# Optimization experiments

Hardware: AMD Instinct MI355X
Metric: run time of the kernel (lower is better)

## Reference

```python
import jax, jax.numpy as jnp
import numpy as np

EPS = 1e-5
AVG_LOG = 1.0  # avg_d['log']
N_NODES = 100000
N_EDGES = 1600000
IN_DIM = 64
EDGE_DIM = 16
OUT_DIM = 64


def setup_inputs() -> dict:
    key = jax.random.key(0)
    ks = jax.random.split(key, 12)
    d_pre_in = 2 * IN_DIM + EDGE_DIM           # 144
    d_post_in = (4 * 3 + 1) * IN_DIM           # 13*64 = 832
    inp = {
        "node_feat": jax.random.normal(ks[0], (N_NODES, IN_DIM), jnp.float32),
        "edge_feat": jax.random.normal(ks[1], (N_EDGES, EDGE_DIM), jnp.float32),
        "pre_W": jax.random.normal(ks[2], (d_pre_in, IN_DIM), jnp.float32) / np.sqrt(d_pre_in),
        "pre_b": jnp.zeros((IN_DIM,), jnp.float32),
        "post_W1": jax.random.normal(ks[3], (d_post_in, OUT_DIM), jnp.float32) / np.sqrt(d_post_in),
        "post_b1": jnp.zeros((OUT_DIM,), jnp.float32),
        "bn_gamma": jnp.ones((OUT_DIM,), jnp.float32),
        "bn_beta": jnp.zeros((OUT_DIM,), jnp.float32),
        "post_W2": jax.random.normal(ks[4], (OUT_DIM, OUT_DIM), jnp.float32) / np.sqrt(OUT_DIM),
        "post_b2": jnp.zeros((OUT_DIM,), jnp.float32),
        "src": jax.random.randint(ks[5], (N_EDGES,), 0, N_NODES, jnp.int32),
        "dst": jax.random.randint(ks[6], (N_EDGES,), 0, N_NODES, jnp.int32),
    }
    return inp


def reference(node_feat, edge_feat, pre_W, pre_b, post_W1, post_b1,
              bn_gamma, bn_beta, post_W2, post_b2, src, dst):
    N = node_feat.shape[0]
    h_in = node_feat

    # --- pretrans edge MLP: cat(h_src, h_dst, e_feat) -> Linear -> relu ---
    z = jnp.concatenate([node_feat[src], node_feat[dst], edge_feat], axis=-1)  # [E, 2D+De]
    e = jax.nn.relu(z @ pre_W + pre_b)                                         # [E, D]

    # --- multi-aggregator neighbor reduction (messages flow src->dst) ---
    deg = jax.ops.segment_sum(jnp.ones((src.shape[0],), e.dtype), dst, num_segments=N)  # [N]
    degc = jnp.maximum(deg, 1.0)[:, None]
    s = jax.ops.segment_sum(e, dst, num_segments=N)
    mean = s / degc
    msq = jax.ops.segment_sum(e * e, dst, num_segments=N) / degc
    var = jax.nn.relu(msq - mean * mean)
    std = jnp.sqrt(var + EPS)
    mx = jax.ops.segment_max(e, dst, num_segments=N)
    mn = jax.ops.segment_min(e, dst, num_segments=N)
    has = (deg > 0)[:, None]
    agg = jnp.concatenate([mean, jnp.where(has, mx, 0.0),
                           jnp.where(has, mn, 0.0), std], axis=-1)  # [N, 4D]
    agg = jnp.where(has, agg, 0.0)  # DGL leaves zero-in-degree nodes zero-filled

    # --- degree scalers: identity, amplification, attenuation ---
    logD = jnp.log(deg + 1.0)[:, None]
    amp = agg * (logD / AVG_LOG)
    att = agg * jnp.where(has, AVG_LOG / jnp.maximum(logD, EPS), 0.0)
    scaled = jnp.concatenate([agg, amp, att], axis=-1)  # [N, 12D]

    # --- posttrans MLP: Linear->relu->BN->Linear->relu, + residual ---
    h = jnp.concatenate([h_in, scaled], axis=-1)        # [N, 13D]
    x = jax.nn.relu(h @ post_W1 + post_b1)
    mu = x.mean(axis=0)
    v = ((x - mu) ** 2).mean(axis=0)
    x = bn_gamma * (x - mu) / jnp.sqrt(v + EPS) + bn_beta
    x = jax.nn.relu(x @ post_W2 + post_b2)
    return x + h_in
```

## Files before the change

kernel.cpp:

```cpp
#include <hip/hip_runtime.h>
#include <math.h>

#define EPSF 1e-5f

typedef __attribute__((ext_vector_type(8))) _Float16 h16x8;
typedef __attribute__((ext_vector_type(4))) float f32x4;
typedef __attribute__((ext_vector_type(4))) unsigned short us4;
typedef __attribute__((ext_vector_type(8))) unsigned short us8;

static __device__ __forceinline__ unsigned short f2h(float f) {
  _Float16 h = (_Float16)f;
  return __builtin_bit_cast(unsigned short, h);
}
static __device__ __forceinline__ float h2f(unsigned short u) {
  _Float16 h = __builtin_bit_cast(_Float16, u);
  return (float)h;
}
static __device__ __forceinline__ int ibcast(int v, int l) {
  return __builtin_amdgcn_readlane(v, l);
}
static __device__ __forceinline__ int lanegather(int v, int srcLane) {
  return __builtin_amdgcn_ds_bpermute(srcLane << 2, v);
}


__global__ __launch_bounds__(256) void k_deg(const int* __restrict__ dst,
                                             int* __restrict__ deg,
                                             int* __restrict__ rank, int E) {
  int i = blockIdx.x * 256 + threadIdx.x;
  if (i < E) rank[i] = atomicAdd(&deg[dst[i]], 1);
}

__global__ __launch_bounds__(1024) void k_scan_a(const int* __restrict__ deg,
                                                 int* __restrict__ offs,
                                                 int* __restrict__ bsum,
                                                 float* __restrict__ aux2, int N) {
  __shared__ int s[1024];
  int t = threadIdx.x;
  int i = blockIdx.x * 1024 + t;
  int v = (i < N) ? deg[i] : 0;
  s[t] = v;
  __syncthreads();
  for (int off = 1; off < 1024; off <<= 1) {
    int x = (t >= off) ? s[t - off] : 0;
    __syncthreads();
    s[t] += x;
    __syncthreads();
  }
  if (i < N) {
    offs[i] = s[t] - v;
    float logD = logf((float)v + 1.f);
    aux2[i * 2] = logD;
    aux2[i * 2 + 1] = (v > 0) ? 1.f / fmaxf(logD, EPSF) : 0.f;
  }
  if (t == 1023) bsum[blockIdx.x] = s[1023];
}

__global__ __launch_bounds__(1024) void k_scan_b(int* __restrict__ bsum, int nb) {
  __shared__ int s[1024];
  int t = threadIdx.x;
  int v = (t < nb) ? bsum[t] : 0;
  s[t] = v;
  __syncthreads();
  for (int off = 1; off < 1024; off <<= 1) {
    int x = (t >= off) ? s[t - off] : 0;
    __syncthreads();
    s[t] += x;
    __syncthreads();
  }
  if (t < nb) bsum[t] = s[t] - v;
}

__global__ __launch_bounds__(1024) void k_scan_c(int* __restrict__ offs,
                                                 const int* __restrict__ bsum,
                                                 int N) {
  int i = blockIdx.x * 1024 + threadIdx.x;
  if (i < N) offs[i] += bsum[blockIdx.x];
}


__global__ __launch_bounds__(256) void k_prep(const float* __restrict__ pre_W,
                                              const float* __restrict__ post_W1,
                                              const float* __restrict__ post_W2,
                                              unsigned short* __restrict__ wsdt,
                                              unsigned short* __restrict__ wt2,
                                              unsigned short* __restrict__ wt3) {
  int idx = blockIdx.x * 256 + threadIdx.x;
  if (idx < 128 * 64) {
    int c = idx >> 6, k = idx & 63;
    float v = (c < 64) ? pre_W[k * 64 + c] : pre_W[(64 + k) * 64 + (c - 64)];
    wsdt[idx] = f2h(v);
  }
  int j = idx - 128 * 64;
  if (j >= 0 && j < 192 * 320) {
    int c = j / 320, k = j - c * 320;
    float v;
    if (c < 64) v = post_W1[k * 64 + c];
    else if (c < 128) v = (k < 64) ? 0.f : post_W1[(256 + k) * 64 + (c - 64)];
    else v = (k < 64) ? 0.f : post_W1[(512 + k) * 64 + (c - 128)];
    wt2[j] = f2h(v);
  }
  int m = idx - 128 * 64 - 192 * 320;
  if (m >= 0 && m < 64 * 64) {
    int c = m >> 6, k = m & 63;
    wt3[m] = f2h(post_W2[k * 64 + c]);
  }
}


__global__ __launch_bounds__(256) void kB_proj(
    const float* __restrict__ nf, const unsigned short* __restrict__ wsdt,
    const float* __restrict__ pre_b, unsigned short* __restrict__ ps,
    unsigned short* __restrict__ pd, int N) {
  __shared__ unsigned short at[64][72];
  int tid = threadIdx.x;
  int n0 = blockIdx.x * 64;
  for (int idx = tid; idx < 64 * 16; idx += 256) {
    int row = idx >> 4, s4 = idx & 15;
    int n = n0 + row;
    us4 o = {0, 0, 0, 0};
    if (n < N) {
      f32x4 v = *(const f32x4*)(nf + (long)n * 64 + s4 * 4);
      o.x = f2h(v.x); o.y = f2h(v.y); o.z = f2h(v.z); o.w = f2h(v.w);
    }
    *(us4*)&at[row][s4 * 4] = o;
    if (s4 < 2) { us4 z = {0, 0, 0, 0}; *(us4*)&at[row][64 + s4 * 4] = z; }
  }
  __syncthreads();
  int lane = tid & 63, w = tid >> 6;
  int r0 = w * 16;
  const unsigned short* ap = &at[r0 + (lane & 15)][(lane >> 4) * 8];
  const unsigned short* bp = wsdt + (lane & 15) * 64 + (lane >> 4) * 8;
  f32x4 acc[8];
#pragma unroll
  for (int c = 0; c < 8; c++) acc[c] = (f32x4){0.f, 0.f, 0.f, 0.f};
#pragma unroll
  for (int c = 0; c < 8; c++) {
#pragma unroll
    for (int kk = 0; kk < 2; kk++) {
      h16x8 a = *(const h16x8*)(ap + kk * 32);
      h16x8 b = *(const h16x8*)(bp + c * 1024 + kk * 32);
      acc[c] = __builtin_amdgcn_mfma_f32_16x16x32_f16(a, b, acc[c], 0, 0, 0);
    }
  }
  int rb = r0 + ((lane >> 4) << 2);
#pragma unroll
  for (int c = 0; c < 8; c++) {
    int col = c * 16 + (lane & 15);
    int cc = col & 63;
    float bv = (col >= 64) ? pre_b[cc] : 0.f;
#pragma unroll
    for (int r = 0; r < 4; r++) {
      int n = n0 + rb + r;
      if (n < N) {
        unsigned short val = f2h(acc[c][r] + bv);
        if (col >= 64) pd[(long)n * 64 + cc] = val;
        else ps[(long)n * 64 + cc] = val;
      }
    }
  }
}


__global__ __launch_bounds__(256) void kQe(
    const float* __restrict__ efeat, const float* __restrict__ pre_W,
    const unsigned short* __restrict__ ps,
    const int* __restrict__ src, const int* __restrict__ dst,
    const int* __restrict__ rank, const int* __restrict__ offs,
    unsigned short* __restrict__ rbuf, int E) {
  __shared__ unsigned short vt[4][16][72];
  int lane = threadIdx.x & 63, w = threadIdx.x >> 6;
  int colb = lane & 15, kg = lane >> 4;

  h16x8 bfrag[4];
#pragma unroll
  for (int ct = 0; ct < 4; ct++) {
    _Float16 tmp[8];
#pragma unroll
    for (int j = 0; j < 8; j++) {
      int k = kg * 8 + j;
      tmp[j] = (k < 16) ? (_Float16)pre_W[(128 + k) * 64 + ct * 16 + colb]
                        : (_Float16)0.f;
    }
    bfrag[ct] = *(h16x8*)tmp;
  }

  const int GROUPS = 4;
  long pbase = ((long)blockIdx.x * 4 + w) * (16 * GROUPS);
#pragma unroll 1
  for (int g = 0; g < GROUPS; g++) {
    long p0 = pbase + (long)g * 16;
    if (p0 >= E) return;

    long pl = p0 + colb;
    int sv = 0, posv = 0;
    if (pl < E) {
      sv = __builtin_nontemporal_load(src + pl);
      int dv = __builtin_nontemporal_load(dst + pl);
      posv = offs[dv] + __builtin_nontemporal_load(rank + pl);
    }

    h16x8 afrag;
    {
      _Float16 tmp[8] = {0, 0, 0, 0, 0, 0, 0, 0};
      if (kg < 2 && pl < E) {
        f32x4 v0 = __builtin_nontemporal_load(
            (const f32x4*)(efeat + pl * 16 + kg * 8));
        f32x4 v1 = __builtin_nontemporal_load(
            (const f32x4*)(efeat + pl * 16 + kg * 8 + 4));
        tmp[0] = (_Float16)v0.x; tmp[1] = (_Float16)v0.y;
        tmp[2] = (_Float16)v0.z; tmp[3] = (_Float16)v0.w;
        tmp[4] = (_Float16)v1.x; tmp[5] = (_Float16)v1.y;
        tmp[6] = (_Float16)v1.z; tmp[7] = (_Float16)v1.w;
      }
      afrag = *(h16x8*)tmp;
    }

    f32x4 acc[4];
#pragma unroll
    for (int ct = 0; ct < 4; ct++) acc[ct] = (f32x4){0.f, 0.f, 0.f, 0.f};
#pragma unroll
    for (int ct = 0; ct < 4; ct++)
      acc[ct] = __builtin_amdgcn_mfma_f32_16x16x32_f16(afrag, bfrag[ct],
                                                       acc[ct], 0, 0, 0);

#pragma unroll
    for (int ct = 0; ct < 4; ct++)
#pragma unroll
      for (int r = 0; r < 4; r++)
        vt[w][kg * 4 + r][ct * 16 + colb] = f2h(acc[ct][r]);

#pragma unroll
    for (int i = 0; i < 16; i++) {
      long p = p0 + i;
      if (p >= E) break;
      int s_i = ibcast(sv, i);
      float v = h2f(vt[w][i][lane]) + h2f(ps[(long)s_i * 64 + lane]);
      vt[w][i][lane] = f2h(v);
    }

#pragma unroll
    for (int pass = 0; pass < 2; pass++) {
      int row = pass * 8 + (lane >> 3);
      long p = p0 + row;
      long pos = (long)lanegather(posv, row);
      if (p < E) {
        us8 val = *(const us8*)&vt[w][row][(lane & 7) * 8];
        *(us8*)(rbuf + pos * 64 + (lane & 7) * 8) = val;
      }
    }
  }
}


__global__ __launch_bounds__(256) void kAgg(
    const unsigned short* __restrict__ rbuf, const unsigned short* __restrict__ pd,
    const int* __restrict__ offs, const int* __restrict__ deg,
    unsigned short* __restrict__ aggb, int N) {
  int lane = threadIdx.x & 63;
  int n = blockIdx.x * 4 + (threadIdx.x >> 6);
  if (n >= N) return;
  int dc = deg[n];
  long ab = (long)n * 256 + lane;
  if (dc == 0) {
    aggb[ab] = 0; aggb[ab + 64] = 0; aggb[ab + 128] = 0; aggb[ab + 192] = 0;
    return;
  }
  float pdv = h2f(pd[(long)n * 64 + lane]);
  long p = offs[n], pe = p + dc;
  float sa = 0.f, qa = 0.f, mx = 0.f, mn = 3.4e38f;
  for (; p + 4 <= pe; p += 4) {
    float v0 = fmaxf(h2f(rbuf[p * 64 + lane]) + pdv, 0.f);
    float v1 = fmaxf(h2f(rbuf[(p + 1) * 64 + lane]) + pdv, 0.f);
    float v2 = fmaxf(h2f(rbuf[(p + 2) * 64 + lane]) + pdv, 0.f);
    float v3 = fmaxf(h2f(rbuf[(p + 3) * 64 + lane]) + pdv, 0.f);
    sa += (v0 + v1) + (v2 + v3);
    qa = fmaf(v0, v0, qa); qa = fmaf(v1, v1, qa);
    qa = fmaf(v2, v2, qa); qa = fmaf(v3, v3, qa);
    mx = fmaxf(mx, fmaxf(fmaxf(v0, v1), fmaxf(v2, v3)));
    mn = fminf(mn, fminf(fminf(v0, v1), fminf(v2, v3)));
  }
  for (; p < pe; p++) {
    float v0 = fmaxf(h2f(rbuf[p * 64 + lane]) + pdv, 0.f);
    sa += v0;
    qa = fmaf(v0, v0, qa);
    mx = fmaxf(mx, v0);
    mn = fminf(mn, v0);
  }
  float invd = 1.f / (float)dc;
  float mean = sa * invd;
  float var = fmaxf(qa * invd - mean * mean, 0.f);
  float stdv = sqrtf(var + EPSF);
  aggb[ab] = f2h(mean);
  aggb[ab + 64] = f2h(mx);
  aggb[ab + 128] = f2h(mn);
  aggb[ab + 192] = f2h(stdv);
}


__global__ __launch_bounds__(256) void kC_post1(
    const float* __restrict__ nf, const unsigned short* __restrict__ aggb,
    const float* __restrict__ aux2, const unsigned short* __restrict__ wt2,
    const float* __restrict__ b1, unsigned short* __restrict__ x1,
    float* __restrict__ bn_sum, float* __restrict__ bn_ssq, int N) {
  __shared__ unsigned short At[64][328];
  int tid = threadIdx.x;
  int n0 = blockIdx.x * 64;
  int lane = tid & 63, w = tid >> 6;
  int colb = lane & 15, kg = lane >> 4;

  const unsigned short* bp0 = wt2 + (long)(w * 16 + colb) * 320 + kg * 8;
  const unsigned short* bp1 = wt2 + (long)(64 + w * 16 + colb) * 320 + kg * 8;
  const unsigned short* bp2 = wt2 + (long)(128 + w * 16 + colb) * 320 + kg * 8;
  h16x8 bf0[10], bf1[8], bf2[8];
#pragma unroll
  for (int kk = 0; kk < 10; kk++) bf0[kk] = *(const h16x8*)(bp0 + kk * 32);
#pragma unroll
  for (int j = 0; j < 8; j++) bf1[j] = *(const h16x8*)(bp1 + (j + 2) * 32);
#pragma unroll
  for (int j = 0; j < 8; j++) bf2[j] = *(const h16x8*)(bp2 + (j + 2) * 32);

  for (int idx = tid; idx < 64 * 40; idx += 256) {
    int row = idx / 40, s = idx - row * 40;
    int n = n0 + row;
    us8 o = {0, 0, 0, 0, 0, 0, 0, 0};
    if (n < N) {
      if (s < 8) {
        f32x4 v0 = *(const f32x4*)(nf + (long)n * 64 + s * 8);
        f32x4 v1 = *(const f32x4*)(nf + (long)n * 64 + s * 8 + 4);
        o[0] = f2h(v0.x); o[1] = f2h(v0.y); o[2] = f2h(v0.z); o[3] = f2h(v0.w);
        o[4] = f2h(v1.x); o[5] = f2h(v1.y); o[6] = f2h(v1.z); o[7] = f2h(v1.w);
      } else {
        o = *((const us8*)(aggb + (long)n * 256) + (s - 8));
      }
    }
    *(us8*)&At[row][s * 8] = o;
  }
  __syncthreads();

  f32x4 acc0[4], acc1[4], acc2[4];
#pragma unroll
  for (int s = 0; s < 4; s++) {
    acc0[s] = (f32x4){0.f, 0.f, 0.f, 0.f};
    acc1[s] = (f32x4){0.f, 0.f, 0.f, 0.f};
    acc2[s] = (f32x4){0.f, 0.f, 0.f, 0.f};
  }
#pragma unroll
  for (int s = 0; s < 4; s++) {
    const unsigned short* ap = &At[s * 16 + colb][kg * 8];
#pragma unroll
    for (int kk = 0; kk < 10; kk++) {
      h16x8 a = *(const h16x8*)(ap + kk * 32);
      acc0[s] = __builtin_amdgcn_mfma_f32_16x16x32_f16(a, bf0[kk], acc0[s], 0, 0, 0);
      if (kk >= 2) {
        acc1[s] = __builtin_amdgcn_mfma_f32_16x16x32_f16(a, bf1[kk - 2], acc1[s], 0, 0, 0);
        acc2[s] = __builtin_amdgcn_mfma_f32_16x16x32_f16(a, bf2[kk - 2], acc2[s], 0, 0, 0);
      }
    }
  }
  __syncthreads();

  float* sx = (float*)&At[0][0];
  int col = w * 16 + colb;
  float bv = b1[col];
#pragma unroll
  for (int s = 0; s < 4; s++) {
    int rb = s * 16 + kg * 4;
#pragma unroll
    for (int r = 0; r < 4; r++) {
      int n = n0 + rb + r;
      float x = 0.f;
      if (n < N) {
        float lg = aux2[(long)n * 2];
        float atf = aux2[(long)n * 2 + 1];
        x = fmaxf(acc0[s][r] + lg * acc1[s][r] + atf * acc2[s][r] + bv, 0.f);
      }
      sx[(rb + r) * 68 + col] = x;
    }
  }
  __syncthreads();

  for (int idx = tid; idx < 64 * 16; idx += 256) {
    int row = idx >> 4, s4 = idx & 15;
    int n = n0 + row;
    if (n < N) {
      const float* p = sx + row * 68 + s4 * 4;
      us4 o;
      o.x = f2h(p[0]); o.y = f2h(p[1]); o.z = f2h(p[2]); o.w = f2h(p[3]);
      *(us4*)(x1 + (long)n * 64 + s4 * 4) = o;
    }
  }
  if (tid < 64) {
    float s = 0.f, s2 = 0.f;
    for (int r = 0; r < 64; r++) {
      float v = sx[r * 68 + tid];
      s += v;
      s2 = fmaf(v, v, s2);
    }
    atomicAdd(&bn_sum[tid], s);
    atomicAdd(&bn_ssq[tid], s2);
  }
}


__global__ __launch_bounds__(64) void k_bnstat(
    const float* __restrict__ bn_sum, const float* __restrict__ bn_ssq,
    const float* __restrict__ gamma, const float* __restrict__ beta,
    float* __restrict__ scale, float* __restrict__ shift, float invN) {
  int j = threadIdx.x;
  float mu = bn_sum[j] * invN;
  float v = fmaxf(bn_ssq[j] * invN - mu * mu, 0.f);
  float sc = gamma[j] / sqrtf(v + EPSF);
  scale[j] = sc;
  shift[j] = beta[j] - mu * sc;
}


__global__ __launch_bounds__(256) void k_post2(
    const unsigned short* __restrict__ x1, const unsigned short* __restrict__ wt3,
    const float* __restrict__ post_b2, const float* __restrict__ scale,
    const float* __restrict__ shift, const float* __restrict__ nf,
    float* __restrict__ out, int N) {
  __shared__ unsigned short at[64][72];
  int tid = threadIdx.x;
  int n0 = blockIdx.x * 64;
  for (int idx = tid; idx < 64 * 16; idx += 256) {
    int row = idx >> 4, s4 = idx & 15;
    int n = n0 + row;
    us4 o = {0, 0, 0, 0};
    if (n < N) {
      us4 xv = *(const us4*)(x1 + (long)n * 64 + s4 * 4);
      f32x4 sc = *(const f32x4*)(scale + s4 * 4);
      f32x4 sh = *(const f32x4*)(shift + s4 * 4);
      o.x = f2h(fmaf(h2f(xv.x), sc.x, sh.x));
      o.y = f2h(fmaf(h2f(xv.y), sc.y, sh.y));
      o.z = f2h(fmaf(h2f(xv.z), sc.z, sh.z));
      o.w = f2h(fmaf(h2f(xv.w), sc.w, sh.w));
    }
    *(us4*)&at[row][s4 * 4] = o;
  }
  __syncthreads();
  int lane = tid & 63, w = tid >> 6;
  int colb = lane & 15, kg = lane >> 4;
  int r0 = w * 16;
  const unsigned short* ap = &at[r0 + colb][kg * 8];
  const unsigned short* bp = wt3 + colb * 64 + kg * 8;
  f32x4 acc[4];
#pragma unroll
  for (int ct = 0; ct < 4; ct++) acc[ct] = (f32x4){0.f, 0.f, 0.f, 0.f};
#pragma unroll
  for (int kk = 0; kk < 2; kk++) {
    h16x8 a = *(const h16x8*)(ap + kk * 32);
#pragma unroll
    for (int ct = 0; ct < 4; ct++) {
      h16x8 b = *(const h16x8*)(bp + ct * (16 * 64) + kk * 32);
      acc[ct] = __builtin_amdgcn_mfma_f32_16x16x32_f16(a, b, acc[ct], 0, 0, 0);
    }
  }
  int rb = r0 + kg * 4;
#pragma unroll
  for (int ct = 0; ct < 4; ct++) {
    int col = ct * 16 + colb;
    float bv = post_b2[col];
#pragma unroll
    for (int r = 0; r < 4; r++) {
      int n = n0 + rb + r;
      if (n < N)
        out[(long)n * 64 + col] =
            fmaxf(acc[ct][r] + bv, 0.f) + nf[(long)n * 64 + col];
    }
  }
}


extern "C" void kernel_launch(void* const* d_in, const int* in_sizes, int n_in,
                              void* d_out, int out_size, void* d_ws, size_t ws_size,
                              hipStream_t stream) {
  const float* node_feat = (const float*)d_in[0];
  const float* edge_feat = (const float*)d_in[1];
  const float* pre_W = (const float*)d_in[2];
  const float* pre_b = (const float*)d_in[3];
  const float* post_W1 = (const float*)d_in[4];
  const float* post_b1 = (const float*)d_in[5];
  const float* bn_gamma = (const float*)d_in[6];
  const float* bn_beta = (const float*)d_in[7];
  const float* post_W2 = (const float*)d_in[8];
  const float* post_b2 = (const float*)d_in[9];
  const int* src = (const int*)d_in[10];
  const int* dst = (const int*)d_in[11];
  float* out = (float*)d_out;

  int N = in_sizes[0] / 64;
  int E = in_sizes[10];

  char* ws = (char*)d_ws;
  size_t off = 0;
  auto alloc = [&](size_t bytes) -> void* {
    void* p = ws + off;
    off += (bytes + 255) & ~(size_t)255;
    return p;
  };
  int* deg = (int*)alloc((size_t)N * 4);
  float* bn_sum = (float*)alloc(64 * 4);
  float* bn_ssq = (float*)alloc(64 * 4);
  size_t zero_span = off;
  int* offs = (int*)alloc((size_t)N * 4);
  int* rank = (int*)alloc((size_t)E * 4);
  int* bsum = (int*)alloc(1024 * 4);
  unsigned short* aggb = (unsigned short*)alloc((size_t)N * 256 * 2);
  float* aux2 = (float*)alloc((size_t)N * 2 * 4);
  unsigned short* psb = (unsigned short*)alloc((size_t)N * 64 * 2);
  unsigned short* pdb = (unsigned short*)alloc((size_t)N * 64 * 2);
  unsigned short* x1 = (unsigned short*)alloc((size_t)N * 64 * 2);
  unsigned short* wsdt = (unsigned short*)alloc(128 * 64 * 2);
  unsigned short* wt2 = (unsigned short*)alloc(192 * 320 * 2);
  unsigned short* wt3 = (unsigned short*)alloc(64 * 64 * 2);
  float* bn_scale = (float*)alloc(64 * 4);
  float* bn_shift = (float*)alloc(64 * 4);
  unsigned short* rbuf = (unsigned short*)alloc((size_t)E * 64 * 2);
  if (off > ws_size) return;

  int nscan = (N + 1023) / 1024;

  hipMemsetAsync(deg, 0, zero_span, stream);
  k_deg<<<(E + 255) / 256, 256, 0, stream>>>(dst, deg, rank, E);
  k_scan_a<<<nscan, 1024, 0, stream>>>(deg, offs, bsum, aux2, N);
  k_scan_b<<<1, 1024, 0, stream>>>(bsum, nscan);
  k_scan_c<<<nscan, 1024, 0, stream>>>(offs, bsum, N);
  k_prep<<<(128 * 64 + 192 * 320 + 64 * 64 + 255) / 256, 256, 0, stream>>>(
      pre_W, post_W1, post_W2, wsdt, wt2, wt3);
  kB_proj<<<(N + 63) / 64, 256, 0, stream>>>(node_feat, wsdt, pre_b, psb, pdb, N);

  kQe<<<(E + 255) / 256, 256, 0, stream>>>(edge_feat, pre_W, psb, src, dst,
                                           rank, offs, rbuf, E);
  kAgg<<<(N + 3) / 4, 256, 0, stream>>>(rbuf, pdb, offs, deg, aggb, N);

  kC_post1<<<(N + 63) / 64, 256, 0, stream>>>(node_feat, aggb, aux2, wt2,
                                              post_b1, x1, bn_sum, bn_ssq, N);

  k_bnstat<<<1, 64, 0, stream>>>(bn_sum, bn_ssq, bn_gamma, bn_beta, bn_scale,
                                 bn_shift, 1.0f / (float)N);

  k_post2<<<(N + 63) / 64, 256, 0, stream>>>(x1, wt3, post_b2, bn_scale,
                                             bn_shift, node_feat, out, N);
}
```

Before: 484.4 us.

## Fuse neighbor aggregation into post-MLP GEMM kernel via shared memory

Merges the per-node multi-aggregator reduction (mean/max/min/std) into the first post-transform GEMM kernel. Each wave now reduces its 16 nodes and writes the aggregates straight into the shared-memory A tile, which removes the fp16 aggb intermediate (N×256 halfs) and one kernel launch. The trade-off is lower parallelism in the reduction phase: 64 nodes per block processed serially per wave, with the block's large LDS footprint and preloaded weight registers limiting occupancy, so gather latency may be less well hidden.

```diff
diff --git a/kernel.cpp b/kernel.cpp
--- a/kernel.cpp
+++ b/kernel.cpp
@@ -253,56 +253,13 @@
 }
 
 
-__global__ __launch_bounds__(256) void kAgg(
-    const unsigned short* __restrict__ rbuf, const unsigned short* __restrict__ pd,
+__global__ __launch_bounds__(256) void kD_fused(
+    const float* __restrict__ nf, const unsigned short* __restrict__ rbuf,
+    const unsigned short* __restrict__ pd, const float* __restrict__ aux2,
+    const unsigned short* __restrict__ wt2, const float* __restrict__ b1,
     const int* __restrict__ offs, const int* __restrict__ deg,
-    unsigned short* __restrict__ aggb, int N) {
-  int lane = threadIdx.x & 63;
-  int n = blockIdx.x * 4 + (threadIdx.x >> 6);
-  if (n >= N) return;
-  int dc = deg[n];
-  long ab = (long)n * 256 + lane;
-  if (dc == 0) {
-    aggb[ab] = 0; aggb[ab + 64] = 0; aggb[ab + 128] = 0; aggb[ab + 192] = 0;
-    return;
-  }
-  float pdv = h2f(pd[(long)n * 64 + lane]);
-  long p = offs[n], pe = p + dc;
-  float sa = 0.f, qa = 0.f, mx = 0.f, mn = 3.4e38f;
-  for (; p + 4 <= pe; p += 4) {
-    float v0 = fmaxf(h2f(rbuf[p * 64 + lane]) + pdv, 0.f);
-    float v1 = fmaxf(h2f(rbuf[(p + 1) * 64 + lane]) + pdv, 0.f);
-    float v2 = fmaxf(h2f(rbuf[(p + 2) * 64 + lane]) + pdv, 0.f);
-    float v3 = fmaxf(h2f(rbuf[(p + 3) * 64 + lane]) + pdv, 0.f);
-    sa += (v0 + v1) + (v2 + v3);
-    qa = fmaf(v0, v0, qa); qa = fmaf(v1, v1, qa);
-    qa = fmaf(v2, v2, qa); qa = fmaf(v3, v3, qa);
-    mx = fmaxf(mx, fmaxf(fmaxf(v0, v1), fmaxf(v2, v3)));
-    mn = fminf(mn, fminf(fminf(v0, v1), fminf(v2, v3)));
-  }
-  for (; p < pe; p++) {
-    float v0 = fmaxf(h2f(rbuf[p * 64 + lane]) + pdv, 0.f);
-    sa += v0;
-    qa = fmaf(v0, v0, qa);
-    mx = fmaxf(mx, v0);
-    mn = fminf(mn, v0);
-  }
-  float invd = 1.f / (float)dc;
-  float mean = sa * invd;
-  float var = fmaxf(qa * invd - mean * mean, 0.f);
-  float stdv = sqrtf(var + EPSF);
-  aggb[ab] = f2h(mean);
-  aggb[ab + 64] = f2h(mx);
-  aggb[ab + 128] = f2h(mn);
-  aggb[ab + 192] = f2h(stdv);
-}
-
-
-__global__ __launch_bounds__(256) void kC_post1(
-    const float* __restrict__ nf, const unsigned short* __restrict__ aggb,
-    const float* __restrict__ aux2, const unsigned short* __restrict__ wt2,
-    const float* __restrict__ b1, unsigned short* __restrict__ x1,
-    float* __restrict__ bn_sum, float* __restrict__ bn_ssq, int N) {
+    unsigned short* __restrict__ x1, float* __restrict__ bn_sum,
+    float* __restrict__ bn_ssq, int N) {
   __shared__ unsigned short At[64][328];
   int tid = threadIdx.x;
   int n0 = blockIdx.x * 64;
@@ -320,21 +277,60 @@
 #pragma unroll
   for (int j = 0; j < 8; j++) bf2[j] = *(const h16x8*)(bp2 + (j + 2) * 32);
 
-  for (int idx = tid; idx < 64 * 40; idx += 256) {
-    int row = idx / 40, s = idx - row * 40;
+  for (int idx = tid; idx < 64 * 8; idx += 256) {
+    int row = idx >> 3, s = idx & 7;
     int n = n0 + row;
     us8 o = {0, 0, 0, 0, 0, 0, 0, 0};
     if (n < N) {
-      if (s < 8) {
-        f32x4 v0 = *(const f32x4*)(nf + (long)n * 64 + s * 8);
-        f32x4 v1 = *(const f32x4*)(nf + (long)n * 64 + s * 8 + 4);
-        o[0] = f2h(v0.x); o[1] = f2h(v0.y); o[2] = f2h(v0.z); o[3] = f2h(v0.w);
-        o[4] = f2h(v1.x); o[5] = f2h(v1.y); o[6] = f2h(v1.z); o[7] = f2h(v1.w);
-      } else {
-        o = *((const us8*)(aggb + (long)n * 256) + (s - 8));
+      f32x4 v0 = *(const f32x4*)(nf + (long)n * 64 + s * 8);
+      f32x4 v1 = *(const f32x4*)(nf + (long)n * 64 + s * 8 + 4);
+      o[0] = f2h(v0.x); o[1] = f2h(v0.y); o[2] = f2h(v0.z); o[3] = f2h(v0.w);
+      o[4] = f2h(v1.x); o[5] = f2h(v1.y); o[6] = f2h(v1.z); o[7] = f2h(v1.w);
+    }
+    *(us8*)&At[row][s * 8] = o;
+  }
+
+#pragma unroll 1
+  for (int i = 0; i < 16; i++) {
+    int row = w * 16 + i;
+    int n = n0 + row;
+    float mean = 0.f, mx = 0.f, mn = 0.f, stdv = 0.f;
+    if (n < N) {
+      int dc = deg[n];
+      if (dc > 0) {
+        float pdv = h2f(pd[(long)n * 64 + lane]);
+        long p = offs[n], pe = p + dc;
+        float sa = 0.f, qa = 0.f, mxr = 0.f, mnr = 3.4e38f;
+        for (; p + 4 <= pe; p += 4) {
+          float v0 = fmaxf(h2f(rbuf[p * 64 + lane]) + pdv, 0.f);
+          float v1 = fmaxf(h2f(rbuf[(p + 1) * 64 + lane]) + pdv, 0.f);
+          float v2 = fmaxf(h2f(rbuf[(p + 2) * 64 + lane]) + pdv, 0.f);
+          float v3 = fmaxf(h2f(rbuf[(p + 3) * 64 + lane]) + pdv, 0.f);
+          sa += (v0 + v1) + (v2 + v3);
+          qa = fmaf(v0, v0, qa); qa = fmaf(v1, v1, qa);
+          qa = fmaf(v2, v2, qa); qa = fmaf(v3, v3, qa);
+          mxr = fmaxf(mxr, fmaxf(fmaxf(v0, v1), fmaxf(v2, v3)));
+          mnr = fminf(mnr, fminf(fminf(v0, v1), fminf(v2, v3)));
+        }
+        for (; p < pe; p++) {
+          float v0 = fmaxf(h2f(rbuf[p * 64 + lane]) + pdv, 0.f);
+          sa += v0;
+          qa = fmaf(v0, v0, qa);
+          mxr = fmaxf(mxr, v0);
+          mnr = fminf(mnr, v0);
+        }
+        float invd = 1.f / (float)dc;
+        mean = sa * invd;
+        float var = fmaxf(qa * invd - mean * mean, 0.f);
+        stdv = sqrtf(var + EPSF);
+        mx = mxr;
+        mn = mnr;
       }
     }
-    *(us8*)&At[row][s * 8] = o;
+    At[row][64 + lane] = f2h(mean);
+    At[row][128 + lane] = f2h(mx);
+    At[row][192 + lane] = f2h(mn);
+    At[row][256 + lane] = f2h(stdv);
   }
   __syncthreads();
 
@@ -507,7 +503,6 @@
   int* offs = (int*)alloc((size_t)N * 4);
   int* rank = (int*)alloc((size_t)E * 4);
   int* bsum = (int*)alloc(1024 * 4);
-  unsigned short* aggb = (unsigned short*)alloc((size_t)N * 256 * 2);
   float* aux2 = (float*)alloc((size_t)N * 2 * 4);
   unsigned short* psb = (unsigned short*)alloc((size_t)N * 64 * 2);
   unsigned short* pdb = (unsigned short*)alloc((size_t)N * 64 * 2);
@@ -533,10 +528,10 @@
 
   kQe<<<(E + 255) / 256, 256, 0, stream>>>(edge_feat, pre_W, psb, src, dst,
                                            rank, offs, rbuf, E);
-  kAgg<<<(N + 3) / 4, 256, 0, stream>>>(rbuf, pdb, offs, deg, aggb, N);
-
-  kC_post1<<<(N + 63) / 64, 256, 0, stream>>>(node_feat, aggb, aux2, wt2,
-                                              post_b1, x1, bn_sum, bn_ssq, N);
+
+  kD_fused<<<(N + 63) / 64, 256, 0, stream>>>(node_feat, rbuf, pdb, aux2, wt2,
+                                              post_b1, offs, deg, x1, bn_sum,
+                                              bn_ssq, N);
 
   k_bnstat<<<1, 64, 0, stream>>>(bn_sum, bn_ssq, bn_gamma, bn_beta, bn_scale,
                                  bn_shift, 1.0f / (float)N);
```

Result: slower. 551.1 us (+13.8%).
